# Optimization experiments

Measured on AMD Instinct MI355X. Metric: run time of the kernel, lower is better.

Reference implementation:

```python
import jax, jax.numpy as jnp
import numpy as np

N_NODES = 100000
N_EMBED = 64
N_HIDDEN = 64
N_EDGES = 1200000


def setup_inputs() -> dict:
    key = jax.random.key(0)
    ks = jax.random.split(key, 8)
    prop_edge_index = jax.random.randint(ks[0], (2, N_EDGES), 0, N_NODES, dtype=jnp.int64)
    emb = jax.random.normal(ks[1], (N_NODES, N_EMBED), dtype=jnp.float32) * 0.05
    # ChebConv K=2 -> two linear weights per layer + bias
    W1_0 = jax.random.normal(ks[2], (N_EMBED, N_HIDDEN), dtype=jnp.float32) * 0.05
    W1_1 = jax.random.normal(ks[3], (N_EMBED, N_HIDDEN), dtype=jnp.float32) * 0.05
    b1 = jnp.zeros((N_HIDDEN,), dtype=jnp.float32)
    W2_0 = jax.random.normal(ks[4], (N_HIDDEN, N_HIDDEN), dtype=jnp.float32) * 0.05
    W2_1 = jax.random.normal(ks[5], (N_HIDDEN, N_HIDDEN), dtype=jnp.float32) * 0.05
    b2 = jnp.zeros((N_HIDDEN,), dtype=jnp.float32)
    return {"prop_edge_index": prop_edge_index, "emb": emb,
            "W1_0": W1_0, "W1_1": W1_1, "b1": b1,
            "W2_0": W2_0, "W2_1": W2_1, "b2": b2}


def _cheb_norm(edge_index, num_nodes):
    """PyG ChebConv.__norm__ with sym normalization, lambda_max=2.0.
    L_hat = 2L/lambda_max - I = (I - D^-1/2 A D^-1/2) - I, so the net
    diagonal weight is 0 and off-diagonal weight is -d_i^-1/2 * d_j^-1/2.
    Self loops in the input are removed first (weight 0)."""
    row, col = edge_index[0], edge_index[1]
    w = jnp.where(row != col, 1.0, 0.0).astype(jnp.float32)  # remove_self_loops
    deg = jax.ops.segment_sum(w, row, num_segments=num_nodes)
    dinv = jnp.where(deg > 0, deg ** -0.5, 0.0)
    norm = -dinv[row] * w * dinv[col]
    return norm


def _cheb_conv(x, src, dst, norm, W0, W1, b, num_nodes):
    # K=2: out = T0(x) @ W0 + T1(x) @ W1 + b, T0 = x, T1 = L_hat x
    Tx1 = jax.ops.segment_sum(norm[:, None] * x[src], dst, num_segments=num_nodes)
    return x @ W0 + Tx1 @ W1 + b


def reference(prop_edge_index, emb, W1_0, W1_1, b1, W2_0, W2_1, b2):
    src, dst = prop_edge_index[0], prop_edge_index[1]
    norm = _cheb_norm(prop_edge_index, N_NODES)
    x = _cheb_conv(emb, src, dst, norm, W1_0, W1_1, b1, N_NODES)
    x = jax.nn.relu(x)
    # dropout: eval mode (identity)
    x = _cheb_conv(x, src, dst, norm, W2_0, W2_1, b2, N_NODES)
    return x
```

## Files before the change

kernel.cpp:

```cpp
#include <hip/hip_runtime.h>

#define N_NODES 100000
#define N_EDGES 1200000
#define NF 64

typedef __attribute__((ext_vector_type(8))) short short8;
typedef __attribute__((ext_vector_type(4))) float float4v;

__device__ __forceinline__ ushort f2bf(float f) {
    unsigned u = __float_as_uint(f);
    return (ushort)((u + 0x7FFF + ((u >> 16) & 1)) >> 16);
}

#define NBINS 391
#define CAP 4352
#define EPB 4096
#define NBLK 293
#define NI4 (N_EDGES / 4)

#define OFF_CNT    0
#define OFF_ENDP   400128
#define OFF_DINV   800256
#define OFF_CUR    1200384
#define OFF_PKW    1203584
#define OFF_SRCS   1236352
#define OFF_SBIN   8042880
#define OFF_DBIN   11446144
#define OFF_EMBBF  18252672
#define OFF_HBF    31052672

__global__ __launch_bounds__(512) void prepsort(const float* __restrict__ W10,
                                                const float* __restrict__ W11,
                                                const float* __restrict__ W20,
                                                const float* __restrict__ W21,
                                                ushort* __restrict__ pk,
                                                const float* __restrict__ emb,
                                                ushort* __restrict__ emb_bf,
                                                const int* __restrict__ row,
                                                const int* __restrict__ col,
                                                int* __restrict__ cur,
                                                ushort* __restrict__ sbinned,
                                                int* __restrict__ dbinned) {
    int b = blockIdx.x;
    int t = threadIdx.x;
    if (b < NBLK) {
        __shared__ int sh[NBINS], dh[NBINS];
        __shared__ int sst[NBINS], dstt[NBINS];
        __shared__ int sgb[NBINS], dgb[NBINS];
        __shared__ int slc[NBINS], dlc[NBINS];
        __shared__ int ssc[512], dsc[512];
        __shared__ ushort sloc[EPB];
        __shared__ int dloc[EPB];
        __shared__ ushort sbid[EPB], dbid[EPB];
        for (int i = t; i < NBINS; i += 512) { sh[i] = 0; dh[i] = 0; }
        __syncthreads();
        int i40 = b * (EPB / 4) + t * 2;
        int4 r0 = make_int4(-1, -1, -1, -1), c0 = r0, r1 = r0, c1 = r0;
        if (i40 < NI4)     { r0 = ((const int4*)row)[i40];     c0 = ((const int4*)col)[i40]; }
        if (i40 + 1 < NI4) { r1 = ((const int4*)row)[i40 + 1]; c1 = ((const int4*)col)[i40 + 1]; }
        int s_[8] = {r0.x, r0.y, r0.z, r0.w, r1.x, r1.y, r1.z, r1.w};
        int d_[8] = {c0.x, c0.y, c0.z, c0.w, c1.x, c1.y, c1.z, c1.w};
#pragma unroll
        for (int j = 0; j < 8; ++j)
            if (s_[j] >= 0 && s_[j] != d_[j]) {
                atomicAdd(&sh[s_[j] >> 8], 1);
                atomicAdd(&dh[d_[j] >> 8], 1);
            }
        __syncthreads();
        int cs = 0, cd = 0;
        if (t < NBINS) {
            cs = sh[t]; cd = dh[t];
            sgb[t] = t * CAP + atomicAdd(&cur[t], cs);
            dgb[t] = t * CAP + atomicAdd(&cur[NBINS + t], cd);
        }
        ssc[t] = (t < NBINS) ? cs : 0;
        dsc[t] = (t < NBINS) ? cd : 0;
        __syncthreads();
        for (int off = 1; off < 512; off <<= 1) {
            int vs = 0, vd = 0;
            if (t >= off) { vs = ssc[t - off]; vd = dsc[t - off]; }
            __syncthreads();
            ssc[t] += vs; dsc[t] += vd;
            __syncthreads();
        }
        if (t < NBINS) {
            sst[t] = ssc[t] - cs; slc[t] = sst[t];
            dstt[t] = dsc[t] - cd; dlc[t] = dstt[t];
        }
        __syncthreads();
#pragma unroll
        for (int j = 0; j < 8; ++j) {
            int s = s_[j], d = d_[j];
            if (s >= 0 && s != d) {
                int sb = s >> 8, db = d >> 8;
                int ls = atomicAdd(&slc[sb], 1);
                sloc[ls] = (ushort)(s & 255); sbid[ls] = (ushort)sb;
                int ld = atomicAdd(&dlc[db], 1);
                dloc[ld] = (s << 8) | (d & 255); dbid[ld] = (ushort)db;
            }
        }
        __syncthreads();
        int totS = ssc[511], totD = dsc[511];
        for (int i = t; i < totS; i += 512) {
            int bi = sbid[i];
            sbinned[sgb[bi] + (i - sst[bi])] = sloc[i];
        }
        for (int i = t; i < totD; i += 512) {
            int bi = dbid[i];
            dbinned[dgb[bi] + (i - dstt[bi])] = dloc[i];
        }
    } else if (b < NBLK + 4) {
        int idx = (b - NBLK) * 512 + t;
        int layer = idx >> 10;
        int rest = idx & 1023;
        int f = rest >> 6, L = rest & 63;
        int n = (f & 3) * 16 + (L & 15);
        int kb = (f >> 2) * 32 + ((L >> 4) << 3);
#pragma unroll
        for (int j = 0; j < 8; ++j) {
            int k = kb + j;
            const float* W = layer ? ((k < 64) ? W20 : W21) : ((k < 64) ? W10 : W11);
            pk[idx * 8 + j] = f2bf(W[(k & 63) * 64 + n]);
        }
    } else {
        int bb = b - NBLK - 4;
        int i = (bb * 512 + t) * 8;
        if (i < N_NODES * NF) {
            float4 v0 = *(const float4*)(emb + i);
            float4 v1 = *(const float4*)(emb + i + 4);
            uint4 o;
            o.x = (uint)f2bf(v0.x) | ((uint)f2bf(v0.y) << 16);
            o.y = (uint)f2bf(v0.z) | ((uint)f2bf(v0.w) << 16);
            o.z = (uint)f2bf(v1.x) | ((uint)f2bf(v1.y) << 16);
            o.w = (uint)f2bf(v1.z) | ((uint)f2bf(v1.w) << 16);
            *(uint4*)(emb_bf + i) = o;
        }
    }
}

__global__ __launch_bounds__(256) void build(const ushort* __restrict__ sbinned,
                                             const int* __restrict__ dbinned,
                                             const int* __restrict__ cur,
                                             float* __restrict__ dinv,
                                             int* __restrict__ cnt,
                                             int* __restrict__ endp,
                                             int* __restrict__ srcs) {
    int t = threadIdx.x;
    int b = blockIdx.x;
    if (b < NBINS) {
        __shared__ int hist[256];
        hist[t] = 0;
        __syncthreads();
        int start = b * CAP;
        int len = cur[b];
        for (int i = t; i < len; i += 256)
            atomicAdd(&hist[sbinned[start + i]], 1);
        __syncthreads();
        int n0 = (b << 8) + t;
        if (n0 < N_NODES) dinv[n0] = hist[t] ? rsqrtf((float)hist[t]) : 0.0f;
    } else {
        int bb = b - NBINS;
        __shared__ int hist[256];
        __shared__ int lcur[256];
        __shared__ int obuf[CAP];
        __shared__ int tot_s;
        hist[t] = 0;
        __syncthreads();
        int start = bb * CAP;
        int len = cur[NBINS + bb];
        for (int i = t; i < len; i += 256)
            atomicAdd(&hist[dbinned[start + i] & 255], 1);
        __syncthreads();
        int o0 = hist[t];
        int A0 = (o0 + 3) & ~3;
        __syncthreads();
        hist[t] = A0;
        __syncthreads();
        for (int off = 1; off < 256; off <<= 1) {
            int v = (t >= off) ? hist[t - off] : 0;
            __syncthreads();
            hist[t] += v;
            __syncthreads();
        }
        int e0 = hist[t] - A0;
        if (t == 255) tot_s = hist[255];
        lcur[t] = e0;
        int n0 = (bb << 8) + t;
        if (n0 < N_NODES) { cnt[n0] = o0; endp[n0] = start + e0 + o0; }
        __syncthreads();
        for (int i = t; i < len; i += 256) {
            int p = dbinned[start + i];
            int slot = atomicAdd(&lcur[p & 255], 1);
            obuf[slot] = p >> 8;
        }
        for (int k = o0; k < A0; ++k) obuf[e0 + k] = 0;
        __syncthreads();
        if (t < 16) obuf[tot_s + t] = 0;
        __syncthreads();
        int tot = tot_s + 16;
        for (int i = t; i < tot; i += 256) srcs[start + i] = obuf[i];
    }
}

#define NPW 16
#define WPB 2
#define NPB (NPW * WPB)
#define LB2 ((N_NODES + NPB - 1) / NPB)

__global__ __launch_bounds__(128, 8) void cheb_layer(const ushort* __restrict__ x,
                                                     const int* __restrict__ srcs,
                                                     const float* __restrict__ dinv,
                                                     const int* __restrict__ endp,
                                                     const int* __restrict__ cnt,
                                                     const ushort* __restrict__ pk,
                                                     const float* __restrict__ bias,
                                                     ushort* __restrict__ out_bf,
                                                     float* __restrict__ out_f32,
                                                     int last) {
    __shared__ ushort sA[WPB][16][136];

    int t = threadIdx.x;
    int lane = t & 63, wid = t >> 6;
    int c = lane & 15, q = lane >> 4;
    int qd = q, fg = c;
    int nb = blockIdx.x * NPB + wid * NPW;

    int nend = 0, ncnt = 0;
    if (lane < NPW && nb + lane < N_NODES) {
        nend = endp[nb + lane];
        ncnt = cnt[nb + lane];
    }

    const uint2* xr = (const uint2*)x;

    auto chunk8 = [&](int eb, int eendL, float& a0, float& a1, float& a2, float& a3) {
        int srcA = srcs[eb + qd];
        int srcB = srcs[eb + 4 + qd];
        float nAf = dinv[srcA];
        float nBf = dinv[srcB];
        nAf = (eb + qd < eendL) ? nAf : 0.0f;
        nBf = (eb + 4 + qd < eendL) ? nBf : 0.0f;
        uint2 gA = xr[(size_t)srcA * 16 + fg];
        uint2 gB = xr[(size_t)srcB * 16 + fg];
        a0 = fmaf(nAf, __uint_as_float(gA.x << 16), a0);
        a1 = fmaf(nAf, __uint_as_float(gA.x & 0xffff0000u), a1);
        a2 = fmaf(nAf, __uint_as_float(gA.y << 16), a2);
        a3 = fmaf(nAf, __uint_as_float(gA.y & 0xffff0000u), a3);
        a0 = fmaf(nBf, __uint_as_float(gB.x << 16), a0);
        a1 = fmaf(nBf, __uint_as_float(gB.x & 0xffff0000u), a1);
        a2 = fmaf(nBf, __uint_as_float(gB.y << 16), a2);
        a3 = fmaf(nBf, __uint_as_float(gB.y & 0xffff0000u), a3);
    };

#pragma unroll
    for (int gp = 0; gp < NPW; gp += 2) {
        int cn0 = __builtin_amdgcn_readlane(ncnt, gp);
        int ee0 = __builtin_amdgcn_readlane(nend, gp);
        int cn1 = __builtin_amdgcn_readlane(ncnt, gp + 1);
        int ee1 = __builtin_amdgcn_readlane(nend, gp + 1);
        int s0 = ee0 - cn0, s1 = ee1 - cn1;
        float a0 = 0, a1 = 0, a2 = 0, a3 = 0;
        float b0 = 0, b1 = 0, b2 = 0, b3 = 0;

        chunk8(s0,     ee0, a0, a1, a2, a3);
        chunk8(s1,     ee1, b0, b1, b2, b3);
        chunk8(s0 + 8, ee0, a0, a1, a2, a3);
        chunk8(s1 + 8, ee1, b0, b1, b2, b3);
        for (int e = s0 + 16; e < ee0; e += 8) chunk8(e, ee0, a0, a1, a2, a3);
        for (int e = s1 + 16; e < ee1; e += 8) chunk8(e, ee1, b0, b1, b2, b3);

        a0 += __shfl_xor(a0, 16, 64); b0 += __shfl_xor(b0, 16, 64);
        a1 += __shfl_xor(a1, 16, 64); b1 += __shfl_xor(b1, 16, 64);
        a2 += __shfl_xor(a2, 16, 64); b2 += __shfl_xor(b2, 16, 64);
        a3 += __shfl_xor(a3, 16, 64); b3 += __shfl_xor(b3, 16, 64);
        a0 += __shfl_xor(a0, 32, 64); b0 += __shfl_xor(b0, 32, 64);
        a1 += __shfl_xor(a1, 32, 64); b1 += __shfl_xor(b1, 32, 64);
        a2 += __shfl_xor(a2, 32, 64); b2 += __shfl_xor(b2, 32, 64);
        a3 += __shfl_xor(a3, 32, 64); b3 += __shfl_xor(b3, 32, 64);

        int node0 = nb + gp, node1 = nb + gp + 1;
        int ni0 = (node0 < N_NODES) ? node0 : 0;
        int ni1 = (node1 < N_NODES) ? node1 : 0;
        if (qd == 0) {
            uint2 xv0 = xr[(size_t)ni0 * 16 + fg];
            uint2 xv1 = xr[(size_t)ni1 * 16 + fg];
            *(uint2*)&sA[wid][gp][4 * fg] = xv0;
            *(uint2*)&sA[wid][gp + 1][4 * fg] = xv1;
        }
        if (qd == 1) {
            float sc0 = -dinv[ni0];
            float sc1 = -dinv[ni1];
            uint2 p0, p1;
            p0.x = (uint)f2bf(a0 * sc0) | ((uint)f2bf(a1 * sc0) << 16);
            p0.y = (uint)f2bf(a2 * sc0) | ((uint)f2bf(a3 * sc0) << 16);
            p1.x = (uint)f2bf(b0 * sc1) | ((uint)f2bf(b1 * sc1) << 16);
            p1.y = (uint)f2bf(b2 * sc1) | ((uint)f2bf(b3 * sc1) << 16);
            *(uint2*)&sA[wid][gp][64 + 4 * fg] = p0;
            *(uint2*)&sA[wid][gp + 1][64 + 4 * fg] = p1;
        }
    }
    __builtin_amdgcn_wave_barrier();

    const short8* pk8 = (const short8*)pk;
    float4v C[4];
#pragma unroll
    for (int nt = 0; nt < 4; ++nt) {
        float b = bias[nt * 16 + c];
        C[nt] = (float4v){b, b, b, b};
    }
#pragma unroll
    for (int kt = 0; kt < 4; ++kt) {
        short8 af = *(const short8*)&sA[wid][c][kt * 32 + q * 8];
#pragma unroll
        for (int nt = 0; nt < 4; ++nt) {
            short8 bfr = pk8[(kt * 4 + nt) * 64 + lane];
            C[nt] = __builtin_amdgcn_mfma_f32_16x16x32_bf16(af, bfr, C[nt], 0, 0, 0);
        }
    }

#pragma unroll
    for (int nt = 0; nt < 4; ++nt) {
#pragma unroll
        for (int i = 0; i < 4; ++i) {
            int node = nb + q * 4 + i;
            if (node < N_NODES) {
                float v = C[nt][i];
                if (!last) {
                    v = fmaxf(v, 0.0f);
                    out_bf[(size_t)node * NF + nt * 16 + c] = f2bf(v);
                } else {
                    out_f32[(size_t)node * NF + nt * 16 + c] = v;
                }
            }
        }
    }
}

extern "C" void kernel_launch(void* const* d_in, const int* in_sizes, int n_in,
                              void* d_out, int out_size, void* d_ws, size_t ws_size,
                              hipStream_t stream) {
    const int* ei = (const int*)d_in[0];
    const int* row = ei;
    const int* col = ei + N_EDGES;
    const float* emb = (const float*)d_in[1];
    const float* W1_0 = (const float*)d_in[2];
    const float* W1_1 = (const float*)d_in[3];
    const float* b1 = (const float*)d_in[4];
    const float* W2_0 = (const float*)d_in[5];
    const float* W2_1 = (const float*)d_in[6];
    const float* b2 = (const float*)d_in[7];
    float* out = (float*)d_out;

    char* ws = (char*)d_ws;
    int* cnt = (int*)(ws + OFF_CNT);
    int* endp = (int*)(ws + OFF_ENDP);
    float* dinv = (float*)(ws + OFF_DINV);
    int* cur = (int*)(ws + OFF_CUR);
    ushort* pk = (ushort*)(ws + OFF_PKW);
    int* srcs = (int*)(ws + OFF_SRCS);
    ushort* sbinned = (ushort*)(ws + OFF_SBIN);
    int* dbinned = (int*)(ws + OFF_DBIN);
    ushort* emb_bf = (ushort*)(ws + OFF_EMBBF);
    ushort* h_bf = (ushort*)(ws + OFF_HBF);

    hipMemsetAsync(cur, 0, 2 * NBINS * sizeof(int), stream);
    prepsort<<<NBLK + 4 + 1563, 512, 0, stream>>>(W1_0, W1_1, W2_0, W2_1, pk,
                                                  emb, emb_bf, row, col, cur,
                                                  sbinned, dbinned);
    build<<<2 * NBINS, 256, 0, stream>>>(sbinned, dbinned, cur, dinv, cnt, endp, srcs);

    cheb_layer<<<LB2, 128, 0, stream>>>(emb_bf, srcs, dinv, endp, cnt, pk, b1, h_bf, nullptr, 0);
    cheb_layer<<<LB2, 128, 0, stream>>>(h_bf, srcs, dinv, endp, cnt, pk + 8192, b2, nullptr, out, 1);
}
```

Before: 188.4 us.

## Pre-scale gathered features by source dinv and process four nodes per pass

Features are stored a second time, already multiplied by each source node's dinv: for the embedding this happens in the build kernel, and for the hidden layer in the first layer's epilogue. The gather loop then drops its per-edge dinv[src] load and only masks out-of-range edges. The aggregation loop also handles four nodes at a time instead of two, giving more independent gathers in flight, and the occupancy hint drops from 8 to 6. The cost is an extra bf16 feature buffer written per layer, and bf16 rounding now happens after scaling, which slightly changes numerics.

```diff
diff --git a/kernel.cpp b/kernel.cpp
--- a/kernel.cpp
+++ b/kernel.cpp
@@ -27,7 +27,9 @@
 #define OFF_SBIN   8042880
 #define OFF_DBIN   11446144
 #define OFF_EMBBF  18252672
-#define OFF_HBF    31052672
+#define OFF_EMBSC  31052672
+#define OFF_HBF    43852672
+#define OFF_HSC    56652672
 
 __global__ __launch_bounds__(512) void prepsort(const float* __restrict__ W10,
                                                 const float* __restrict__ W11,
@@ -141,7 +143,9 @@
 __global__ __launch_bounds__(256) void build(const ushort* __restrict__ sbinned,
                                              const int* __restrict__ dbinned,
                                              const int* __restrict__ cur,
+                                             const float* __restrict__ emb,
                                              float* __restrict__ dinv,
+                                             ushort* __restrict__ emb_sc,
                                              int* __restrict__ cnt,
                                              int* __restrict__ endp,
                                              int* __restrict__ srcs) {
@@ -149,6 +153,7 @@
     int b = blockIdx.x;
     if (b < NBINS) {
         __shared__ int hist[256];
+        __shared__ float dvs[256];
         hist[t] = 0;
         __syncthreads();
         int start = b * CAP;
@@ -157,7 +162,26 @@
             atomicAdd(&hist[sbinned[start + i]], 1);
         __syncthreads();
         int n0 = (b << 8) + t;
-        if (n0 < N_NODES) dinv[n0] = hist[t] ? rsqrtf((float)hist[t]) : 0.0f;
+        float dv = hist[t] ? rsqrtf((float)hist[t]) : 0.0f;
+        if (n0 < N_NODES) dinv[n0] = dv;
+        dvs[t] = dv;
+        __syncthreads();
+        size_t base4 = ((size_t)b << 8) * 16;
+        const float4* ef = (const float4*)emb;
+        uint2* es = (uint2*)emb_sc;
+#pragma unroll
+        for (int k = 0; k < 16; ++k) {
+            int l = k * 256 + t;
+            size_t gi = base4 + l;
+            if (gi < (size_t)N_NODES * 16) {
+                float4 v = ef[gi];
+                float sc = dvs[l >> 4];
+                uint2 o;
+                o.x = (uint)f2bf(v.x * sc) | ((uint)f2bf(v.y * sc) << 16);
+                o.y = (uint)f2bf(v.z * sc) | ((uint)f2bf(v.w * sc) << 16);
+                es[gi] = o;
+            }
+        }
     } else {
         int bb = b - NBINS;
         __shared__ int hist[256];
@@ -207,7 +231,8 @@
 #define NPB (NPW * WPB)
 #define LB2 ((N_NODES + NPB - 1) / NPB)
 
-__global__ __launch_bounds__(128, 8) void cheb_layer(const ushort* __restrict__ x,
+__global__ __launch_bounds__(128, 6) void cheb_layer(const ushort* __restrict__ x,
+                                                     const ushort* __restrict__ xs,
                                                      const int* __restrict__ srcs,
                                                      const float* __restrict__ dinv,
                                                      const int* __restrict__ endp,
@@ -215,6 +240,7 @@
                                                      const ushort* __restrict__ pk,
                                                      const float* __restrict__ bias,
                                                      ushort* __restrict__ out_bf,
+                                                     ushort* __restrict__ out_sc,
                                                      float* __restrict__ out_f32,
                                                      int last) {
     __shared__ ushort sA[WPB][16][136];
@@ -232,71 +258,103 @@
     }
 
     const uint2* xr = (const uint2*)x;
+    const uint2* xsr = (const uint2*)xs;
 
     auto chunk8 = [&](int eb, int eendL, float& a0, float& a1, float& a2, float& a3) {
         int srcA = srcs[eb + qd];
         int srcB = srcs[eb + 4 + qd];
-        float nAf = dinv[srcA];
-        float nBf = dinv[srcB];
-        nAf = (eb + qd < eendL) ? nAf : 0.0f;
-        nBf = (eb + 4 + qd < eendL) ? nBf : 0.0f;
-        uint2 gA = xr[(size_t)srcA * 16 + fg];
-        uint2 gB = xr[(size_t)srcB * 16 + fg];
-        a0 = fmaf(nAf, __uint_as_float(gA.x << 16), a0);
-        a1 = fmaf(nAf, __uint_as_float(gA.x & 0xffff0000u), a1);
-        a2 = fmaf(nAf, __uint_as_float(gA.y << 16), a2);
-        a3 = fmaf(nAf, __uint_as_float(gA.y & 0xffff0000u), a3);
-        a0 = fmaf(nBf, __uint_as_float(gB.x << 16), a0);
-        a1 = fmaf(nBf, __uint_as_float(gB.x & 0xffff0000u), a1);
-        a2 = fmaf(nBf, __uint_as_float(gB.y << 16), a2);
-        a3 = fmaf(nBf, __uint_as_float(gB.y & 0xffff0000u), a3);
+        float mA = (eb + qd < eendL) ? 1.0f : 0.0f;
+        float mB = (eb + 4 + qd < eendL) ? 1.0f : 0.0f;
+        uint2 gA = xsr[(size_t)srcA * 16 + fg];
+        uint2 gB = xsr[(size_t)srcB * 16 + fg];
+        a0 = fmaf(mA, __uint_as_float(gA.x << 16), a0);
+        a1 = fmaf(mA, __uint_as_float(gA.x & 0xffff0000u), a1);
+        a2 = fmaf(mA, __uint_as_float(gA.y << 16), a2);
+        a3 = fmaf(mA, __uint_as_float(gA.y & 0xffff0000u), a3);
+        a0 = fmaf(mB, __uint_as_float(gB.x << 16), a0);
+        a1 = fmaf(mB, __uint_as_float(gB.x & 0xffff0000u), a1);
+        a2 = fmaf(mB, __uint_as_float(gB.y << 16), a2);
+        a3 = fmaf(mB, __uint_as_float(gB.y & 0xffff0000u), a3);
     };
 
 #pragma unroll
-    for (int gp = 0; gp < NPW; gp += 2) {
-        int cn0 = __builtin_amdgcn_readlane(ncnt, gp);
-        int ee0 = __builtin_amdgcn_readlane(nend, gp);
-        int cn1 = __builtin_amdgcn_readlane(ncnt, gp + 1);
-        int ee1 = __builtin_amdgcn_readlane(nend, gp + 1);
-        int s0 = ee0 - cn0, s1 = ee1 - cn1;
+    for (int gp = 0; gp < NPW; gp += 4) {
+        int cnA = __builtin_amdgcn_readlane(ncnt, gp);
+        int eeA = __builtin_amdgcn_readlane(nend, gp);
+        int cnB = __builtin_amdgcn_readlane(ncnt, gp + 1);
+        int eeB = __builtin_amdgcn_readlane(nend, gp + 1);
+        int cnC = __builtin_amdgcn_readlane(ncnt, gp + 2);
+        int eeC = __builtin_amdgcn_readlane(nend, gp + 2);
+        int cnD = __builtin_amdgcn_readlane(ncnt, gp + 3);
+        int eeD = __builtin_amdgcn_readlane(nend, gp + 3);
+        int sA0 = eeA - cnA, sB0 = eeB - cnB, sC0 = eeC - cnC, sD0 = eeD - cnD;
         float a0 = 0, a1 = 0, a2 = 0, a3 = 0;
         float b0 = 0, b1 = 0, b2 = 0, b3 = 0;
-
-        chunk8(s0,     ee0, a0, a1, a2, a3);
-        chunk8(s1,     ee1, b0, b1, b2, b3);
-        chunk8(s0 + 8, ee0, a0, a1, a2, a3);
-        chunk8(s1 + 8, ee1, b0, b1, b2, b3);
-        for (int e = s0 + 16; e < ee0; e += 8) chunk8(e, ee0, a0, a1, a2, a3);
-        for (int e = s1 + 16; e < ee1; e += 8) chunk8(e, ee1, b0, b1, b2, b3);
+        float c0 = 0, c1 = 0, c2 = 0, c3 = 0;
+        float d0 = 0, d1 = 0, d2 = 0, d3 = 0;
+
+        chunk8(sA0,     eeA, a0, a1, a2, a3);
+        chunk8(sB0,     eeB, b0, b1, b2, b3);
+        chunk8(sC0,     eeC, c0, c1, c2, c3);
+        chunk8(sD0,     eeD, d0, d1, d2, d3);
+        chunk8(sA0 + 8, eeA, a0, a1, a2, a3);
+        chunk8(sB0 + 8, eeB, b0, b1, b2, b3);
+        chunk8(sC0 + 8, eeC, c0, c1, c2, c3);
+        chunk8(sD0 + 8, eeD, d0, d1, d2, d3);
+        for (int e = sA0 + 16; e < eeA; e += 8) chunk8(e, eeA, a0, a1, a2, a3);
+        for (int e = sB0 + 16; e < eeB; e += 8) chunk8(e, eeB, b0, b1, b2, b3);
+        for (int e = sC0 + 16; e < eeC; e += 8) chunk8(e, eeC, c0, c1, c2, c3);
+        for (int e = sD0 + 16; e < eeD; e += 8) chunk8(e, eeD, d0, d1, d2, d3);
 
         a0 += __shfl_xor(a0, 16, 64); b0 += __shfl_xor(b0, 16, 64);
+        c0 += __shfl_xor(c0, 16, 64); d0 += __shfl_xor(d0, 16, 64);
         a1 += __shfl_xor(a1, 16, 64); b1 += __shfl_xor(b1, 16, 64);
+        c1 += __shfl_xor(c1, 16, 64); d1 += __shfl_xor(d1, 16, 64);
         a2 += __shfl_xor(a2, 16, 64); b2 += __shfl_xor(b2, 16, 64);
+        c2 += __shfl_xor(c2, 16, 64); d2 += __shfl_xor(d2, 16, 64);
         a3 += __shfl_xor(a3, 16, 64); b3 += __shfl_xor(b3, 16, 64);
+        c3 += __shfl_xor(c3, 16, 64); d3 += __shfl_xor(d3, 16, 64);
         a0 += __shfl_xor(a0, 32, 64); b0 += __shfl_xor(b0, 32, 64);
+        c0 += __shfl_xor(c0, 32, 64); d0 += __shfl_xor(d0, 32, 64);
         a1 += __shfl_xor(a1, 32, 64); b1 += __shfl_xor(b1, 32, 64);
+        c1 += __shfl_xor(c1, 32, 64); d1 += __shfl_xor(d1, 32, 64);
         a2 += __shfl_xor(a2, 32, 64); b2 += __shfl_xor(b2, 32, 64);
+        c2 += __shfl_xor(c2, 32, 64); d2 += __shfl_xor(d2, 32, 64);
         a3 += __shfl_xor(a3, 32, 64); b3 += __shfl_xor(b3, 32, 64);
-
-        int node0 = nb + gp, node1 = nb + gp + 1;
-        int ni0 = (node0 < N_NODES) ? node0 : 0;
-        int ni1 = (node1 < N_NODES) ? node1 : 0;
+        c3 += __shfl_xor(c3, 32, 64); d3 += __shfl_xor(d3, 32, 64);
+
+        int ni0 = (nb + gp     < N_NODES) ? (nb + gp)     : 0;
+        int ni1 = (nb + gp + 1 < N_NODES) ? (nb + gp + 1) : 0;
+        int ni2 = (nb + gp + 2 < N_NODES) ? (nb + gp + 2) : 0;
+        int ni3 = (nb + gp + 3 < N_NODES) ? (nb + gp + 3) : 0;
         if (qd == 0) {
             uint2 xv0 = xr[(size_t)ni0 * 16 + fg];
             uint2 xv1 = xr[(size_t)ni1 * 16 + fg];
+            uint2 xv2 = xr[(size_t)ni2 * 16 + fg];
+            uint2 xv3 = xr[(size_t)ni3 * 16 + fg];
             *(uint2*)&sA[wid][gp][4 * fg] = xv0;
             *(uint2*)&sA[wid][gp + 1][4 * fg] = xv1;
+            *(uint2*)&sA[wid][gp + 2][4 * fg] = xv2;
+            *(uint2*)&sA[wid][gp + 3][4 * fg] = xv3;
         }
         if (qd == 1) {
             float sc0 = -dinv[ni0];
             float sc1 = -dinv[ni1];
-            uint2 p0, p1;
+            float sc2 = -dinv[ni2];
+            float sc3 = -dinv[ni3];
+            uint2 p0, p1, p2, p3;
             p0.x = (uint)f2bf(a0 * sc0) | ((uint)f2bf(a1 * sc0) << 16);
             p0.y = (uint)f2bf(a2 * sc0) | ((uint)f2bf(a3 * sc0) << 16);
             p1.x = (uint)f2bf(b0 * sc1) | ((uint)f2bf(b1 * sc1) << 16);
             p1.y = (uint)f2bf(b2 * sc1) | ((uint)f2bf(b3 * sc1) << 16);
+            p2.x = (uint)f2bf(c0 * sc2) | ((uint)f2bf(c1 * sc2) << 16);
+            p2.y = (uint)f2bf(c2 * sc2) | ((uint)f2bf(c3 * sc2) << 16);
+            p3.x = (uint)f2bf(d0 * sc3) | ((uint)f2bf(d1 * sc3) << 16);
+            p3.y = (uint)f2bf(d2 * sc3) | ((uint)f2bf(d3 * sc3) << 16);
             *(uint2*)&sA[wid][gp][64 + 4 * fg] = p0;
             *(uint2*)&sA[wid][gp + 1][64 + 4 * fg] = p1;
+            *(uint2*)&sA[wid][gp + 2][64 + 4 * fg] = p2;
+            *(uint2*)&sA[wid][gp + 3][64 + 4 * fg] = p3;
         }
     }
     __builtin_amdgcn_wave_barrier();
@@ -318,6 +376,14 @@
         }
     }
 
+    float dvv[4];
+    if (!last) {
+#pragma unroll
+        for (int i = 0; i < 4; ++i) {
+            int node = nb + q * 4 + i;
+            dvv[i] = (node < N_NODES) ? dinv[node] : 0.0f;
+        }
+    }
 #pragma unroll
     for (int nt = 0; nt < 4; ++nt) {
 #pragma unroll
@@ -328,6 +394,7 @@
                 if (!last) {
                     v = fmaxf(v, 0.0f);
                     out_bf[(size_t)node * NF + nt * 16 + c] = f2bf(v);
+                    out_sc[(size_t)node * NF + nt * 16 + c] = f2bf(v * dvv[i]);
                 } else {
                     out_f32[(size_t)node * NF + nt * 16 + c] = v;
                 }
@@ -361,14 +428,19 @@
     ushort* sbinned = (ushort*)(ws + OFF_SBIN);
     int* dbinned = (int*)(ws + OFF_DBIN);
     ushort* emb_bf = (ushort*)(ws + OFF_EMBBF);
+    ushort* emb_sc = (ushort*)(ws + OFF_EMBSC);
     ushort* h_bf = (ushort*)(ws + OFF_HBF);
+    ushort* h_sc = (ushort*)(ws + OFF_HSC);
 
     hipMemsetAsync(cur, 0, 2 * NBINS * sizeof(int), stream);
     prepsort<<<NBLK + 4 + 1563, 512, 0, stream>>>(W1_0, W1_1, W2_0, W2_1, pk,
                                                   emb, emb_bf, row, col, cur,
                                                   sbinned, dbinned);
-    build<<<2 * NBINS, 256, 0, stream>>>(sbinned, dbinned, cur, dinv, cnt, endp, srcs);
-
-    cheb_layer<<<LB2, 128, 0, stream>>>(emb_bf, srcs, dinv, endp, cnt, pk, b1, h_bf, nullptr, 0);
-    cheb_layer<<<LB2, 128, 0, stream>>>(h_bf, srcs, dinv, endp, cnt, pk + 8192, b2, nullptr, out, 1);
+    build<<<2 * NBINS, 256, 0, stream>>>(sbinned, dbinned, cur, emb, dinv, emb_sc,
+                                         cnt, endp, srcs);
+
+    cheb_layer<<<LB2, 128, 0, stream>>>(emb_bf, emb_sc, srcs, dinv, endp, cnt,
+                                        pk, b1, h_bf, h_sc, nullptr, 0);
+    cheb_layer<<<LB2, 128, 0, stream>>>(h_bf, h_sc, srcs, dinv, endp, cnt,
+                                        pk + 8192, b2, nullptr, nullptr, out, 1);
 }
```

After: 196.9 us. 1.04x slower.

## Split Cheb layer into feature-blocked gather and separate MFMA matmul kernels

Applied to the files above, without the earlier changes.

Node features are stored in a feature-blocked layout (four 16-feature slabs of 32 bytes per node), so each aggregation block gathers only one slab. The goal is a smaller gather footprint per pass that fits better in cache. The fused aggregate-plus-MFMA kernel becomes two kernels: agg writes the normalized neighbour sum to a bf16 buffer, and mm loads x and Tx to run the MFMA. The trade-off is extra kernel launches, a round trip of Tx through global memory, and the index and dinv loads being repeated for each of the four feature blocks.

```diff
diff --git a/kernel.cpp b/kernel.cpp
--- a/kernel.cpp
+++ b/kernel.cpp
@@ -26,8 +26,9 @@
 #define OFF_SRCS   1236352
 #define OFF_SBIN   8042880
 #define OFF_DBIN   11446144
-#define OFF_EMBBF  18252672
-#define OFF_HBF    31052672
+#define OFF_X4     18252672
+#define OFF_H4     31052672
+#define OFF_TX     43852672
 
 __global__ __launch_bounds__(512) void prepsort(const float* __restrict__ W10,
                                                 const float* __restrict__ W11,
@@ -35,7 +36,7 @@
                                                 const float* __restrict__ W21,
                                                 ushort* __restrict__ pk,
                                                 const float* __restrict__ emb,
-                                                ushort* __restrict__ emb_bf,
+                                                ushort* __restrict__ x4,
                                                 const int* __restrict__ row,
                                                 const int* __restrict__ col,
                                                 int* __restrict__ cur,
@@ -133,7 +134,8 @@
             o.y = (uint)f2bf(v0.z) | ((uint)f2bf(v0.w) << 16);
             o.z = (uint)f2bf(v1.x) | ((uint)f2bf(v1.y) << 16);
             o.w = (uint)f2bf(v1.z) | ((uint)f2bf(v1.w) << 16);
-            *(uint4*)(emb_bf + i) = o;
+            int n = i >> 6, f0 = i & 63, fb = f0 >> 4;
+            *(uint4*)(x4 + ((size_t)fb * N_NODES + n) * 16 + (f0 & 15)) = o;
         }
     }
 }
@@ -202,58 +204,52 @@
     }
 }
 
-#define NPW 16
-#define WPB 2
-#define NPB (NPW * WPB)
-#define LB2 ((N_NODES + NPB - 1) / NPB)
-
-__global__ __launch_bounds__(128, 8) void cheb_layer(const ushort* __restrict__ x,
-                                                     const int* __restrict__ srcs,
-                                                     const float* __restrict__ dinv,
-                                                     const int* __restrict__ endp,
-                                                     const int* __restrict__ cnt,
-                                                     const ushort* __restrict__ pk,
-                                                     const float* __restrict__ bias,
-                                                     ushort* __restrict__ out_bf,
-                                                     float* __restrict__ out_f32,
-                                                     int last) {
-    __shared__ ushort sA[WPB][16][136];
-
+#define ANPW 16
+#define AWPB 2
+#define ANPB 32
+#define ANG  3125
+#define AGRID 12504
+
+__global__ __launch_bounds__(128, 6) void agg(const ushort* __restrict__ xt,
+                                              const int* __restrict__ srcs,
+                                              const float* __restrict__ dinv,
+                                              const int* __restrict__ endp,
+                                              const int* __restrict__ cnt,
+                                              ushort* __restrict__ tx) {
+    int bid = blockIdx.x;
+    int r = bid & 7;
+    int fb = r >> 1;
+    int ng = (bid >> 3) * 2 + (r & 1);
+    if (ng >= ANG) return;
     int t = threadIdx.x;
     int lane = t & 63, wid = t >> 6;
-    int c = lane & 15, q = lane >> 4;
-    int qd = q, fg = c;
-    int nb = blockIdx.x * NPB + wid * NPW;
+    int es = lane >> 2;
+    int k = lane & 3;
+    int nb = ng * ANPB + wid * ANPW;
 
     int nend = 0, ncnt = 0;
-    if (lane < NPW && nb + lane < N_NODES) {
+    if (lane < ANPW && nb + lane < N_NODES) {
         nend = endp[nb + lane];
         ncnt = cnt[nb + lane];
     }
 
-    const uint2* xr = (const uint2*)x;
-
-    auto chunk8 = [&](int eb, int eendL, float& a0, float& a1, float& a2, float& a3) {
-        int srcA = srcs[eb + qd];
-        int srcB = srcs[eb + 4 + qd];
-        float nAf = dinv[srcA];
-        float nBf = dinv[srcB];
-        nAf = (eb + qd < eendL) ? nAf : 0.0f;
-        nBf = (eb + 4 + qd < eendL) ? nBf : 0.0f;
-        uint2 gA = xr[(size_t)srcA * 16 + fg];
-        uint2 gB = xr[(size_t)srcB * 16 + fg];
-        a0 = fmaf(nAf, __uint_as_float(gA.x << 16), a0);
-        a1 = fmaf(nAf, __uint_as_float(gA.x & 0xffff0000u), a1);
-        a2 = fmaf(nAf, __uint_as_float(gA.y << 16), a2);
-        a3 = fmaf(nAf, __uint_as_float(gA.y & 0xffff0000u), a3);
-        a0 = fmaf(nBf, __uint_as_float(gB.x << 16), a0);
-        a1 = fmaf(nBf, __uint_as_float(gB.x & 0xffff0000u), a1);
-        a2 = fmaf(nBf, __uint_as_float(gB.y << 16), a2);
-        a3 = fmaf(nBf, __uint_as_float(gB.y & 0xffff0000u), a3);
+    const uint2* xb = (const uint2*)xt + (size_t)fb * N_NODES * 4;
+    uint2* txb = (uint2*)tx + (size_t)fb * N_NODES * 4;
+
+    auto chunk16 = [&](int eb, int ee, float& a0, float& a1, float& a2, float& a3) {
+        int e = eb + es;
+        int v = srcs[e];
+        float nv = dinv[v];
+        nv = (e < ee) ? nv : 0.0f;
+        uint2 g = xb[(size_t)v * 4 + k];
+        a0 = fmaf(nv, __uint_as_float(g.x << 16), a0);
+        a1 = fmaf(nv, __uint_as_float(g.x & 0xffff0000u), a1);
+        a2 = fmaf(nv, __uint_as_float(g.y << 16), a2);
+        a3 = fmaf(nv, __uint_as_float(g.y & 0xffff0000u), a3);
     };
 
 #pragma unroll
-    for (int gp = 0; gp < NPW; gp += 2) {
+    for (int gp = 0; gp < ANPW; gp += 2) {
         int cn0 = __builtin_amdgcn_readlane(ncnt, gp);
         int ee0 = __builtin_amdgcn_readlane(nend, gp);
         int cn1 = __builtin_amdgcn_readlane(ncnt, gp + 1);
@@ -262,13 +258,19 @@
         float a0 = 0, a1 = 0, a2 = 0, a3 = 0;
         float b0 = 0, b1 = 0, b2 = 0, b3 = 0;
 
-        chunk8(s0,     ee0, a0, a1, a2, a3);
-        chunk8(s1,     ee1, b0, b1, b2, b3);
-        chunk8(s0 + 8, ee0, a0, a1, a2, a3);
-        chunk8(s1 + 8, ee1, b0, b1, b2, b3);
-        for (int e = s0 + 16; e < ee0; e += 8) chunk8(e, ee0, a0, a1, a2, a3);
-        for (int e = s1 + 16; e < ee1; e += 8) chunk8(e, ee1, b0, b1, b2, b3);
-
+        chunk16(s0, ee0, a0, a1, a2, a3);
+        chunk16(s1, ee1, b0, b1, b2, b3);
+        for (int e = s0 + 16; e < ee0; e += 16) chunk16(e, ee0, a0, a1, a2, a3);
+        for (int e = s1 + 16; e < ee1; e += 16) chunk16(e, ee1, b0, b1, b2, b3);
+
+        a0 += __shfl_xor(a0, 4, 64);  b0 += __shfl_xor(b0, 4, 64);
+        a1 += __shfl_xor(a1, 4, 64);  b1 += __shfl_xor(b1, 4, 64);
+        a2 += __shfl_xor(a2, 4, 64);  b2 += __shfl_xor(b2, 4, 64);
+        a3 += __shfl_xor(a3, 4, 64);  b3 += __shfl_xor(b3, 4, 64);
+        a0 += __shfl_xor(a0, 8, 64);  b0 += __shfl_xor(b0, 8, 64);
+        a1 += __shfl_xor(a1, 8, 64);  b1 += __shfl_xor(b1, 8, 64);
+        a2 += __shfl_xor(a2, 8, 64);  b2 += __shfl_xor(b2, 8, 64);
+        a3 += __shfl_xor(a3, 8, 64);  b3 += __shfl_xor(b3, 8, 64);
         a0 += __shfl_xor(a0, 16, 64); b0 += __shfl_xor(b0, 16, 64);
         a1 += __shfl_xor(a1, 16, 64); b1 += __shfl_xor(b1, 16, 64);
         a2 += __shfl_xor(a2, 16, 64); b2 += __shfl_xor(b2, 16, 64);
@@ -278,25 +280,60 @@
         a2 += __shfl_xor(a2, 32, 64); b2 += __shfl_xor(b2, 32, 64);
         a3 += __shfl_xor(a3, 32, 64); b3 += __shfl_xor(b3, 32, 64);
 
-        int node0 = nb + gp, node1 = nb + gp + 1;
-        int ni0 = (node0 < N_NODES) ? node0 : 0;
-        int ni1 = (node1 < N_NODES) ? node1 : 0;
-        if (qd == 0) {
-            uint2 xv0 = xr[(size_t)ni0 * 16 + fg];
-            uint2 xv1 = xr[(size_t)ni1 * 16 + fg];
-            *(uint2*)&sA[wid][gp][4 * fg] = xv0;
-            *(uint2*)&sA[wid][gp + 1][4 * fg] = xv1;
-        }
-        if (qd == 1) {
-            float sc0 = -dinv[ni0];
-            float sc1 = -dinv[ni1];
-            uint2 p0, p1;
-            p0.x = (uint)f2bf(a0 * sc0) | ((uint)f2bf(a1 * sc0) << 16);
-            p0.y = (uint)f2bf(a2 * sc0) | ((uint)f2bf(a3 * sc0) << 16);
-            p1.x = (uint)f2bf(b0 * sc1) | ((uint)f2bf(b1 * sc1) << 16);
-            p1.y = (uint)f2bf(b2 * sc1) | ((uint)f2bf(b3 * sc1) << 16);
-            *(uint2*)&sA[wid][gp][64 + 4 * fg] = p0;
-            *(uint2*)&sA[wid][gp + 1][64 + 4 * fg] = p1;
+        int n0 = nb + gp, n1 = nb + gp + 1;
+        if (lane < 4 && n0 < N_NODES) {
+            float sc = -dinv[n0];
+            uint2 p;
+            p.x = (uint)f2bf(a0 * sc) | ((uint)f2bf(a1 * sc) << 16);
+            p.y = (uint)f2bf(a2 * sc) | ((uint)f2bf(a3 * sc) << 16);
+            txb[(size_t)n0 * 4 + k] = p;
+        }
+        if (lane >= 4 && lane < 8 && n1 < N_NODES) {
+            float sc = -dinv[n1];
+            uint2 p;
+            p.x = (uint)f2bf(b0 * sc) | ((uint)f2bf(b1 * sc) << 16);
+            p.y = (uint)f2bf(b2 * sc) | ((uint)f2bf(b3 * sc) << 16);
+            txb[(size_t)n1 * 4 + k] = p;
+        }
+    }
+}
+
+#define NPW 16
+#define WPB 2
+#define NPB (NPW * WPB)
+#define LB2 ((N_NODES + NPB - 1) / NPB)
+
+__global__ __launch_bounds__(128, 6) void mm(const ushort* __restrict__ x4,
+                                             const ushort* __restrict__ tx,
+                                             const ushort* __restrict__ pk,
+                                             const float* __restrict__ bias,
+                                             ushort* __restrict__ out_h4,
+                                             float* __restrict__ out_f32,
+                                             int last) {
+    __shared__ ushort sA[WPB][16][136];
+
+    int t = threadIdx.x;
+    int lane = t & 63, wid = t >> 6;
+    int c = lane & 15, q = lane >> 4;
+    int nb = blockIdx.x * NPB + wid * NPW;
+
+    const uint2* xu = (const uint2*)x4;
+    const uint2* tu = (const uint2*)tx;
+    int fbx = c >> 2, j = c & 3;
+
+#pragma unroll
+    for (int gp = 0; gp < NPW; gp += 2) {
+        int ni0 = (nb + gp < N_NODES) ? (nb + gp) : 0;
+        int ni1 = (nb + gp + 1 < N_NODES) ? (nb + gp + 1) : 0;
+        size_t o0 = ((size_t)fbx * N_NODES + ni0) * 4 + j;
+        size_t o1 = ((size_t)fbx * N_NODES + ni1) * 4 + j;
+        if (q == 0) {
+            *(uint2*)&sA[wid][gp][4 * c] = xu[o0];
+            *(uint2*)&sA[wid][gp + 1][4 * c] = xu[o1];
+        }
+        if (q == 1) {
+            *(uint2*)&sA[wid][gp][64 + 4 * c] = tu[o0];
+            *(uint2*)&sA[wid][gp + 1][64 + 4 * c] = tu[o1];
         }
     }
     __builtin_amdgcn_wave_barrier();
@@ -327,7 +364,7 @@
                 float v = C[nt][i];
                 if (!last) {
                     v = fmaxf(v, 0.0f);
-                    out_bf[(size_t)node * NF + nt * 16 + c] = f2bf(v);
+                    out_h4[((size_t)nt * N_NODES + node) * 16 + c] = f2bf(v);
                 } else {
                     out_f32[(size_t)node * NF + nt * 16 + c] = v;
                 }
@@ -360,15 +397,18 @@
     int* srcs = (int*)(ws + OFF_SRCS);
     ushort* sbinned = (ushort*)(ws + OFF_SBIN);
     int* dbinned = (int*)(ws + OFF_DBIN);
-    ushort* emb_bf = (ushort*)(ws + OFF_EMBBF);
-    ushort* h_bf = (ushort*)(ws + OFF_HBF);
+    ushort* x4 = (ushort*)(ws + OFF_X4);
+    ushort* h4 = (ushort*)(ws + OFF_H4);
+    ushort* tx = (ushort*)(ws + OFF_TX);
 
     hipMemsetAsync(cur, 0, 2 * NBINS * sizeof(int), stream);
     prepsort<<<NBLK + 4 + 1563, 512, 0, stream>>>(W1_0, W1_1, W2_0, W2_1, pk,
-                                                  emb, emb_bf, row, col, cur,
+                                                  emb, x4, row, col, cur,
                                                   sbinned, dbinned);
     build<<<2 * NBINS, 256, 0, stream>>>(sbinned, dbinned, cur, dinv, cnt, endp, srcs);
 
-    cheb_layer<<<LB2, 128, 0, stream>>>(emb_bf, srcs, dinv, endp, cnt, pk, b1, h_bf, nullptr, 0);
-    cheb_layer<<<LB2, 128, 0, stream>>>(h_bf, srcs, dinv, endp, cnt, pk + 8192, b2, nullptr, out, 1);
-}
+    agg<<<AGRID, 128, 0, stream>>>(x4, srcs, dinv, endp, cnt, tx);
+    mm<<<LB2, 128, 0, stream>>>(x4, tx, pk, b1, h4, nullptr, 0);
+    agg<<<AGRID, 128, 0, stream>>>(h4, srcs, dinv, endp, cnt, tx);
+    mm<<<LB2, 128, 0, stream>>>(h4, tx, pk + 8192, b2, nullptr, out, 1);
+}
```

Measured after the change: 302.5 us. +60.6%, slower.
